# Performance work log

Hardware: AMD Instinct MI355X
Metric: run time of the kernel (lower is better)

Reference implementation:

```python
import jax, jax.numpy as jnp
import numpy as np

OUT_SIZE = 7          # pooled output H=W
SPATIAL_SCALE = 0.125 # FPN stride 8
SAMPLE_NUM = 2        # sampling grid per bin (static)
N_ORIENT = 8
PI = 3.141592653589793


def setup_inputs() -> dict:
    key = jax.random.key(0)
    k1, k2, k3, k4, k5 = jax.random.split(key, 5)
    features = jax.random.normal(k1, (2, 256, 256, 256), dtype=jnp.float32)
    R = 512
    batch = jax.random.randint(k2, (R,), 0, 2).astype(jnp.float32)
    centers = jax.random.uniform(k3, (R, 2), minval=64.0, maxval=1984.0)
    wh = jax.random.uniform(k4, (R, 2), minval=32.0, maxval=512.0)
    theta = jax.random.uniform(k5, (R, 1), minval=0.0, maxval=2.0 * PI)
    rois = jnp.concatenate([batch[:, None], centers, wh, theta], axis=1)
    return {"features": features, "rois": rois}


def _riroi_align(features, rois):
    B, Ctot, H, W = features.shape
    O = N_ORIENT
    C = Ctot // O
    P, G = OUT_SIZE, SAMPLE_NUM
    dtype = features.dtype
    Rn = rois.shape[0]

    batch_ind = rois[:, 0].astype(jnp.int32)
    cw = rois[:, 1] * SPATIAL_SCALE
    ch = rois[:, 2] * SPATIAL_SCALE
    rw = jnp.maximum(rois[:, 3] * SPATIAL_SCALE, 1.0)
    rh = jnp.maximum(rois[:, 4] * SPATIAL_SCALE, 1.0)
    theta = rois[:, 5]

    # orientation alignment: interpolate between two circularly-shifted channels
    ind_f = theta * O / (2.0 * PI)
    ind_floor = jnp.floor(ind_f)
    l_var = ind_f - ind_floor          # weight on shifted-plus-one plane
    r_var = 1.0 - l_var
    ind = jnp.mod(ind_floor.astype(jnp.int32), O)
    o_idx = jnp.arange(O, dtype=jnp.int32)
    ind_rot = jnp.mod(o_idx[None, :] - ind[:, None], O)   # [R,O]
    ind_rot_p = jnp.mod(ind_rot + 1, O)

    # rotated sampling grid; layout (ph, iy, pw, ix) flattened to S
    bin_h = rh / P
    bin_w = rw / P
    pidx = jnp.arange(P, dtype=dtype)
    gidx = (jnp.arange(G, dtype=dtype) + 0.5) / G
    yy = -rh[:, None, None] / 2.0 + (pidx[None, :, None] + gidx[None, None, :]) * bin_h[:, None, None]  # [R,P,G]
    xx = -rw[:, None, None] / 2.0 + (pidx[None, :, None] + gidx[None, None, :]) * bin_w[:, None, None]
    yy = yy[:, :, :, None, None]          # [R,P,G,1,1]
    xx = xx[:, None, None, :, :]          # [R,1,1,P,G]
    cos_t = jnp.cos(theta)[:, None, None, None, None]
    sin_t = jnp.sin(theta)[:, None, None, None, None]
    x = (xx * cos_t - yy * sin_t + cw[:, None, None, None, None]).reshape(Rn, -1)  # [R,S]
    y = (xx * sin_t + yy * cos_t + ch[:, None, None, None, None]).reshape(Rn, -1)
    S = x.shape[1]

    # bilinear interpolation corner indices/weights (ROIAlign semantics)
    valid = (y > -1.0) & (y < H) & (x > -1.0) & (x < W)
    yc = jnp.clip(y, 0.0, None)
    xc = jnp.clip(x, 0.0, None)
    y_low = yc.astype(jnp.int32)
    x_low = xc.astype(jnp.int32)
    y_edge = y_low >= H - 1
    x_edge = x_low >= W - 1
    y_high = jnp.where(y_edge, H - 1, y_low + 1)
    x_high = jnp.where(x_edge, W - 1, x_low + 1)
    y_low = jnp.where(y_edge, H - 1, y_low)
    x_low = jnp.where(x_edge, W - 1, x_low)
    yv = jnp.where(y_edge, y_low.astype(dtype), yc)
    xv = jnp.where(x_edge, x_low.astype(dtype), xc)
    ly = yv - y_low.astype(dtype)
    lx = xv - x_low.astype(dtype)
    hy = 1.0 - ly
    hx = 1.0 - lx
    vm = valid.astype(dtype)
    w00 = hy * hx * vm
    w01 = hy * lx * vm
    w10 = ly * hx * vm
    w11 = ly * lx * vm

    # [B,O,H,W,C] so the channel dim is gathered contiguously
    feats = features.reshape(B, C, O, H, W).transpose(0, 2, 3, 4, 1)
    b = batch_ind[:, None, None]  # [R,1,1]
    yl = y_low[:, None, :]
    yh = y_high[:, None, :]
    xl = x_low[:, None, :]
    xh = x_high[:, None, :]

    def gather_plane(plane):  # plane [R,O] -> [R,O,S,C]
        p = plane[:, :, None]
        return (w00[:, None, :, None] * feats[b, p, yl, xl]
                + w01[:, None, :, None] * feats[b, p, yl, xh]
                + w10[:, None, :, None] * feats[b, p, yh, xl]
                + w11[:, None, :, None] * feats[b, p, yh, xh])

    val = gather_plane(ind_rot)
    val_p = gather_plane(ind_rot_p)
    out = r_var[:, None, None, None] * val + l_var[:, None, None, None] * val_p  # [R,O,S,C]
    out = out.reshape(Rn, O, P, G, P, G, C).mean(axis=(3, 5))  # average over bin samples
    out = out.transpose(0, 4, 1, 2, 3).reshape(Rn, C * O, P, P)  # channel layout c*O + o
    return out


def reference(features, rois):
    return _riroi_align(features, rois)
```

## Files before the change

kernel.cpp:

```cpp
#include <hip/hip_runtime.h>


#include <hip/hip_fp16.h>

typedef _Float16 h16;
typedef _Float16 h8 __attribute__((ext_vector_type(8)));

#define NS 196
#define HW 65536
#define TWO_PI_F 6.283185307179586f
#define OPITCH 260
#define TP 40

__global__ __launch_bounds__(256) void transpose_kernel(
    const float* __restrict__ in, h16* __restrict__ out)
{
    __shared__ h16 lds[256 * TP];
    const int t = threadIdx.x;
    const int a = t & 63;
    const int w = t >> 6;

    const int b  = blockIdx.z;
    const int tc = blockIdx.y;
    const int tp = blockIdx.x;

    const float* ip = in + ((size_t)b * 256 + tc * 32 + w * 8) * HW + tp * 256 + a * 4;

    float4 v[8];
    #pragma unroll
    for (int j = 0; j < 8; ++j)
        v[j] = *(const float4*)(ip + (size_t)j * HW);

    #pragma unroll
    for (int p = 0; p < 4; ++p) {
        h8 row;
        #pragma unroll
        for (int j = 0; j < 8; ++j)
            row[j] = (h16)(((const float*)&v[j])[p]);
        *(h8*)&lds[(a * 4 + p) * TP + w * 8] = row;
    }
    __syncthreads();

    h16* op = out + ((size_t)b * HW + (size_t)tp * 256) * 256 + tc * 32;
    #pragma unroll
    for (int k = 0; k < 4; ++k) {
        int px   = (t >> 2) + k * 64;
        int part = t & 3;
        h8 r = *(const h8*)&lds[px * TP + part * 8];
        *(h8*)(op + (size_t)px * 256 + part * 8) = r;
    }
}

__global__ __launch_bounds__(1024, 8) void riroi_gather(
    const h16* __restrict__ ft, const float* __restrict__ rois,
    float* __restrict__ out)
{
    const int r = blockIdx.x;
    const int tid  = threadIdx.x;
    const int lane = tid & 63;
    const int wave = tid >> 6;
    const int l32  = lane & 31;
    const int hi   = lane >> 5;

    const float* roi = rois + r * 6;
    const int   b  = (int)roi[0];
    const float cw = roi[1] * 0.125f;
    const float ch = roi[2] * 0.125f;
    const float rw = fmaxf(roi[3] * 0.125f, 1.0f);
    const float rh = fmaxf(roi[4] * 0.125f, 1.0f);
    const float theta = roi[5];

    const float ind_f = theta * 8.0f / TWO_PI_F;
    const float fl    = floorf(ind_f);
    const float lvar  = ind_f - fl;
    const float rvar  = 1.0f - lvar;
    int ii = (int)fl;
    const int ind = ((ii % 8) + 8) & 7;

    const float cost = cosf(theta), sint = sinf(theta);
    const float bin_h = rh / 7.0f, bin_w = rw / 7.0f;

    __shared__ int   s_off[4][NS];
    __shared__ float s_w[4][NS];
    __shared__ float s_out[49 * OPITCH];

    if (tid < NS) {
        int iy = tid / 14, ix = tid - iy * 14;
        int py = iy >> 1, gy = iy & 1;
        int px = ix >> 1, gx = ix & 1;
        float yy = ((float)py + ((float)gy + 0.5f) * 0.5f) * bin_h - rh * 0.5f;
        float xx = ((float)px + ((float)gx + 0.5f) * 0.5f) * bin_w - rw * 0.5f;
        float x = xx * cost - yy * sint + cw;
        float y = xx * sint + yy * cost + ch;
        float vm = (y > -1.0f && y < 256.0f && x > -1.0f && x < 256.0f) ? 1.0f : 0.0f;
        float yc = fmaxf(y, 0.0f), xc = fmaxf(x, 0.0f);
        int y0 = (int)yc, x0 = (int)xc;
        int y1, x1; float yv, xv;
        if (y0 >= 255) { y0 = 255; y1 = 255; yv = 255.0f; }
        else           { y1 = y0 + 1; yv = yc; }
        if (x0 >= 255) { x0 = 255; x1 = 255; xv = 255.0f; }
        else           { x1 = x0 + 1; xv = xc; }
        float ly = yv - (float)y0, lx = xv - (float)x0;
        float hy = 1.0f - ly, hx = 1.0f - lx;
        s_w[0][tid] = hy * hx * vm;
        s_w[1][tid] = hy * lx * vm;
        s_w[2][tid] = ly * hx * vm;
        s_w[3][tid] = ly * lx * vm;
        int y0w = y0 << 8, y1w = y1 << 8;
        s_off[0][tid] = y0w + x0;
        s_off[1][tid] = y0w + x1;
        s_off[2][tid] = y1w + x0;
        s_off[3][tid] = y1w + x1;
    }
    __syncthreads();

    const h16* fb = ft + (size_t)b * ((size_t)HW * 256) + (l32 << 3);

    for (int bin = wave; bin < 49; bin += 16) {
        int py = bin / 7, px = bin - py * 7;
        int sbase = py * 28 + px * 2;
        float v[8] = {0.f, 0.f, 0.f, 0.f, 0.f, 0.f, 0.f, 0.f};
        #pragma unroll
        for (int k = 0; k < 4; ++k) {
            int s = sbase + ((k & 1) ? 1 : 0) + ((k & 2) ? 14 : 0);
            #pragma unroll
            for (int cnp = 0; cnp < 2; ++cnp) {
                int   cn  = cnp * 2 + hi;
                int   o   = s_off[cn][s];
                float wgt = s_w[cn][s];
                h8 f = *(const h8*)(fb + (size_t)o * 256);
                #pragma unroll
                for (int i = 0; i < 8; ++i)
                    v[i] += wgt * (float)f[i];
            }
        }
        #pragma unroll
        for (int i = 0; i < 8; ++i)
            v[i] += __shfl_xor(v[i], 32);

        if (hi == 0) {
            float res[8];
            #pragma unroll
            for (int i = 0; i < 8; ++i)
                res[i] = 0.25f * (rvar * v[i] + lvar * v[(i + 1) & 7]);
            float* dst = &s_out[bin * OPITCH + (l32 << 3)];
            *(float4*)dst       = make_float4(res[0], res[1], res[2], res[3]);
            *(float4*)(dst + 4) = make_float4(res[4], res[5], res[6], res[7]);
        }
    }
    __syncthreads();

    const int ind_neg = (8 - ind) & 7;
    float* ob = out + (size_t)r * 12544;
    for (int i = tid << 2; i < 12544; i += 4096) {
        float4 vo;
        #pragma unroll
        for (int q = 0; q < 4; ++q) {
            int j   = i + q;
            int co  = j / 49;
            int bin = j - co * 49;
            int ci  = (co & ~7) | ((co + ind_neg) & 7);
            ((float*)&vo)[q] = s_out[bin * OPITCH + ci];
        }
        *(float4*)(ob + i) = vo;
    }
}

extern "C" void kernel_launch(void* const* d_in, const int* in_sizes, int n_in,
                              void* d_out, int out_size, void* d_ws, size_t ws_size,
                              hipStream_t stream) {
    const float* feat = (const float*)d_in[0];
    const float* rois = (const float*)d_in[1];
    float* out = (float*)d_out;

    h16* ft = (h16*)d_ws;
    transpose_kernel<<<dim3(256, 8, 2), dim3(256), 0, stream>>>(feat, ft);
    riroi_gather<<<dim3(512), dim3(1024), 0, stream>>>(ft, rois, out);
}
```

Before: 251.0 us.

## Split each ROI across two blocks by channel half, four corners per wave

The gather kernel now launches two 512-thread blocks per ROI, each handling 128 of the 256 channels, in place of one 1024-thread block. Within a wave, the four bilinear corners go to separate 16-lane groups and are summed with two xor shuffles, replacing two corner loads per lane. Precomputed offsets now include the channel pitch, and the output staging buffer shrinks to match. Both blocks of a ROI redo the sampling-grid setup, which adds some duplicated work, but the smaller blocks give the scheduler more freedom and use less LDS each.

```diff
diff --git a/kernel.cpp b/kernel.cpp
--- a/kernel.cpp
+++ b/kernel.cpp
@@ -1,7 +1,6 @@
 #include <hip/hip_runtime.h>
+#include <hip/hip_fp16.h>
 
-
-#include <hip/hip_fp16.h>
 
 typedef _Float16 h16;
 typedef _Float16 h8 __attribute__((ext_vector_type(8)));
@@ -9,7 +8,7 @@
 #define NS 196
 #define HW 65536
 #define TWO_PI_F 6.283185307179586f
-#define OPITCH 260
+#define OPITCH 132
 #define TP 40
 
 __global__ __launch_bounds__(256) void transpose_kernel(
@@ -51,16 +50,17 @@
     }
 }
 
-__global__ __launch_bounds__(1024, 8) void riroi_gather(
+__global__ __launch_bounds__(512, 8) void riroi_gather(
     const h16* __restrict__ ft, const float* __restrict__ rois,
     float* __restrict__ out)
 {
-    const int r = blockIdx.x;
+    const int r    = blockIdx.x >> 1;
+    const int half = blockIdx.x & 1;
     const int tid  = threadIdx.x;
     const int lane = tid & 63;
     const int wave = tid >> 6;
-    const int l32  = lane & 31;
-    const int hi   = lane >> 5;
+    const int cn   = lane >> 4;
+    const int chg  = lane & 15;
 
     const float* roi = rois + r * 6;
     const int   b  = (int)roi[0];
@@ -107,43 +107,40 @@
         s_w[2][tid] = ly * hx * vm;
         s_w[3][tid] = ly * lx * vm;
         int y0w = y0 << 8, y1w = y1 << 8;
-        s_off[0][tid] = y0w + x0;
-        s_off[1][tid] = y0w + x1;
-        s_off[2][tid] = y1w + x0;
-        s_off[3][tid] = y1w + x1;
+        s_off[0][tid] = (y0w + x0) << 8;
+        s_off[1][tid] = (y0w + x1) << 8;
+        s_off[2][tid] = (y1w + x0) << 8;
+        s_off[3][tid] = (y1w + x1) << 8;
     }
     __syncthreads();
 
-    const h16* fb = ft + (size_t)b * ((size_t)HW * 256) + (l32 << 3);
+    const h16* fb = ft + (size_t)b * ((size_t)HW * 256) + half * 128 + (chg << 3);
 
-    for (int bin = wave; bin < 49; bin += 16) {
+    for (int bin = wave; bin < 49; bin += 8) {
         int py = bin / 7, px = bin - py * 7;
         int sbase = py * 28 + px * 2;
         float v[8] = {0.f, 0.f, 0.f, 0.f, 0.f, 0.f, 0.f, 0.f};
         #pragma unroll
         for (int k = 0; k < 4; ++k) {
-            int s = sbase + ((k & 1) ? 1 : 0) + ((k & 2) ? 14 : 0);
+            int   s   = sbase + (k & 1) + ((k & 2) ? 14 : 0);
+            int   o   = s_off[cn][s];
+            float wgt = s_w[cn][s];
+            h8 f = *(const h8*)(fb + o);
             #pragma unroll
-            for (int cnp = 0; cnp < 2; ++cnp) {
-                int   cn  = cnp * 2 + hi;
-                int   o   = s_off[cn][s];
-                float wgt = s_w[cn][s];
-                h8 f = *(const h8*)(fb + (size_t)o * 256);
-                #pragma unroll
-                for (int i = 0; i < 8; ++i)
-                    v[i] += wgt * (float)f[i];
-            }
+            for (int i = 0; i < 8; ++i)
+                v[i] += wgt * (float)f[i];
         }
         #pragma unroll
-        for (int i = 0; i < 8; ++i)
+        for (int i = 0; i < 8; ++i) {
+            v[i] += __shfl_xor(v[i], 16);
             v[i] += __shfl_xor(v[i], 32);
-
-        if (hi == 0) {
+        }
+        if (cn == 0) {
             float res[8];
             #pragma unroll
             for (int i = 0; i < 8; ++i)
                 res[i] = 0.25f * (rvar * v[i] + lvar * v[(i + 1) & 7]);
-            float* dst = &s_out[bin * OPITCH + (l32 << 3)];
+            float* dst = &s_out[bin * OPITCH + (chg << 3)];
             *(float4*)dst       = make_float4(res[0], res[1], res[2], res[3]);
             *(float4*)(dst + 4) = make_float4(res[4], res[5], res[6], res[7]);
         }
@@ -151,8 +148,8 @@
     __syncthreads();
 
     const int ind_neg = (8 - ind) & 7;
-    float* ob = out + (size_t)r * 12544;
-    for (int i = tid << 2; i < 12544; i += 4096) {
+    float* ob = out + (size_t)r * 12544 + half * 6272;
+    for (int i = tid << 2; i < 6272; i += 2048) {
         float4 vo;
         #pragma unroll
         for (int q = 0; q < 4; ++q) {
@@ -175,5 +172,5 @@
 
     h16* ft = (h16*)d_ws;
     transpose_kernel<<<dim3(256, 8, 2), dim3(256), 0, stream>>>(feat, ft);
-    riroi_gather<<<dim3(512), dim3(1024), 0, stream>>>(ft, rois, out);
+    riroi_gather<<<dim3(1024), dim3(512), 0, stream>>>(ft, rois, out);
 }
```

Result: no change. 248.9 us (-0.8%).
